# Kernel tuning notes

Measured on AMD Instinct MI355X. Metric: run time of the kernel, lower is better.

## Reference

```python
import jax, jax.numpy as jnp
import numpy as np

# --- dims (match init_kwargs) ---
H = 2048      # hidden_dim
NH = 16       # num_heads
QL = 1536     # q_latent_dim
KVL = 512     # kv_latent_dim
QR = 64       # q_rope_dim (== k_rope_dim)
QN = 128      # q_nope_dim
KR = 64       # k_rope_dim
KN = 128      # k_nope_dim
VD = 128      # v_dim
B, S = 1, 2048
BASE = 10000.0
EPS = 1e-6


def rms_norm(x, w, eps=EPS):
    xf = x.astype(jnp.float32)
    var = jnp.mean(xf * xf, axis=-1, keepdims=True)
    return w * (xf * jax.lax.rsqrt(var + eps)).astype(x.dtype)


def rope_cos_sin(seq_len, dim, base=BASE):
    inv_freq = 1.0 / (base ** (jnp.arange(0, dim, 2, dtype=jnp.float32) / dim))
    t = jnp.arange(seq_len, dtype=jnp.float32)
    freqs = jnp.outer(t, inv_freq)
    emb = jnp.concatenate([freqs, freqs], axis=-1)  # [S, dim]
    return jnp.cos(emb), jnp.sin(emb)


def rotate_half(x):
    d = x.shape[-1] // 2
    return jnp.concatenate([-x[..., d:], x[..., :d]], axis=-1)


def apply_rotary_pos_emb(q, k, cos, sin, position_ids):
    # cos/sin: [S, d]; position_ids: [B, S] -> [B, 1, S, d]
    cos = cos[position_ids][:, None]
    sin = sin[position_ids][:, None]

    def interleave(x):  # matches view(b,h,s,d//2,2).transpose(4,3).reshape
        b, h, s, d = x.shape
        return x.reshape(b, h, s, d // 2, 2).transpose(0, 1, 2, 4, 3).reshape(b, h, s, d)

    q = interleave(q)
    k = interleave(k)
    return q * cos + rotate_half(q) * sin, k * cos + rotate_half(k) * sin


def setup_inputs() -> dict:
    key = jax.random.key(0)
    ks = jax.random.split(key, 8)
    sc = 0.02
    hidden_states = jax.random.normal(ks[0], (B, S, H), dtype=jnp.float32)
    position_ids = jnp.broadcast_to(jnp.arange(S, dtype=jnp.int32), (B, S))
    attn_mask = jnp.tril(jnp.ones((S, S), dtype=jnp.int32))[None, None]  # causal, [1,1,S,S]
    return {
        "hidden_states": hidden_states,
        "position_ids": position_ids,
        "attn_mask": attn_mask,
        "q_down_w": jax.random.normal(ks[1], (QL, H), jnp.float32) * sc,
        "kv_down_w": jax.random.normal(ks[2], (KVL + KR, H), jnp.float32) * sc,
        "q_up_w": jax.random.normal(ks[3], (NH * (QN + QR), QL), jnp.float32) * sc,
        "k_up_w": jax.random.normal(ks[4], (NH * (KN + VD), KVL), jnp.float32) * sc,
        "o_w": jax.random.normal(ks[5], (H, NH * VD), jnp.float32) * sc,
        "q_norm_w": jnp.ones((QL,), jnp.float32),
        "kv_norm_w": jnp.ones((KVL + KR,), jnp.float32),
    }


def reference(hidden_states, position_ids, attn_mask, q_down_w, kv_down_w,
              q_up_w, k_up_w, o_w, q_norm_w, kv_norm_w):
    bsz, seq_len, _ = hidden_states.shape

    # --- query path: down-proj -> RMSNorm -> up-proj ---
    latent_cq = rms_norm(hidden_states @ q_down_w.T, q_norm_w)        # [B,S,QL]
    q = latent_cq @ q_up_w.T                                          # [B,S,NH*(QN+QR)]
    q = q.reshape(bsz, seq_len, NH, QN + QR).transpose(0, 2, 1, 3)    # [B,NH,S,QN+QR]
    q_nope, q_pe = q[..., :QN], q[..., QN:]

    # --- kv path: down-proj -> RMSNorm -> split latent / shared k_pe ---
    compressed_kv = rms_norm(hidden_states @ kv_down_w.T, kv_norm_w)  # [B,S,KVL+KR]
    latent_ckv, k_pe = compressed_kv[..., :KVL], compressed_kv[..., KVL:]
    kv = latent_ckv @ k_up_w.T                                        # [B,S,NH*(KN+VD)]
    kv = kv.reshape(bsz, seq_len, NH, KN + VD).transpose(0, 2, 1, 3)  # [B,NH,S,KN+VD]
    k_nope, value = kv[..., :KN], kv[..., KN:]

    # --- partial RoPE on rotary sub-dims ---
    cos, sin = rope_cos_sin(seq_len, QR)
    k_pe = k_pe[:, None]                                              # [B,1,S,KR] shared across heads
    q_rope, k_rope = apply_rotary_pos_emb(q_pe, k_pe, cos, sin, position_ids)
    k_rope = jnp.broadcast_to(k_rope, (bsz, NH, seq_len, KR))

    query = jnp.concatenate([q_rope, q_nope], axis=-1)                # [B,NH,S,QR+QN]
    key = jnp.concatenate([k_rope, k_nope], axis=-1)                  # [B,NH,S,KR+KN]

    # --- explicit attention (no 1/sqrt(d) scale, matching the source) ---
    attn_weights = jnp.einsum('bhqd,bhkd->bhqk', query, key)
    attn_weights = jnp.where(attn_mask == 0, -jnp.inf, attn_weights)
    attn_weights = jax.nn.softmax(attn_weights, axis=-1)
    attn_output = jnp.einsum('bhqk,bhkd->bhqd', attn_weights, value)
    attn_output = attn_output.transpose(0, 2, 1, 3).reshape(bsz, seq_len, NH * VD)
    attn_output = attn_output @ o_w.T                                 # [B,S,H]
    return attn_weights, attn_output
```

## Files before the change

### kernel.cpp

```cpp
#include <hip/hip_runtime.h>
#include <cstdint>
#include <cmath>

typedef _Float16 f16;
using f16x8 = __attribute__((ext_vector_type(8))) _Float16;
using f16x4 = __attribute__((ext_vector_type(4))) _Float16;
using f32x4 = __attribute__((ext_vector_type(4))) float;

#define NHEAD 16
#define SEQ   2048
#define KSS   4
#define NEG_INF -3.0e38f

static __device__ __forceinline__ f32x4 mfma16(f16x8 a, f16x8 b, f32x4 c) {
    return __builtin_amdgcn_mfma_f32_16x16x32_f16(a, b, c, 0, 0, 0);
}

static __device__ __forceinline__ void gload16(const void* gp, void* lp) {
    __builtin_amdgcn_global_load_lds(
        (const __attribute__((address_space(1))) unsigned int*)gp,
        (__attribute__((address_space(3))) unsigned int*)lp, 16, 0, 0);
}

__global__ __launch_bounds__(256) void k_cvt_all(
    const float* __restrict__ hsrc, const float* __restrict__ qdw, const float* __restrict__ kvdw,
    const float* __restrict__ quw, const float* __restrict__ kuw, const float* __restrict__ ow,
    f16* __restrict__ h16, f16* __restrict__ dw16, f16* __restrict__ quw16,
    f16* __restrict__ kuw16, f16* __restrict__ ow16, float* __restrict__ cs)
{
    constexpr int C1 = 1048576;
    constexpr int C2 = C1 + 786432;
    constexpr int C3 = C2 + 327680;
    constexpr int C4 = C3 + 1179648;
    constexpr int C5 = C4 + 524288;
    constexpr int C6 = C5 + 1048576;
    int chunk = blockIdx.x * 256 + threadIdx.x;
    if (chunk >= C6) {
        int idx = chunk - C6;
        if (idx < 65536) {
            int t = idx >> 5, j = idx & 31;
            float invf = (float)pow(10000.0, -(double)j / 32.0);
            float ang  = (float)t * invf;
            cs[t * 64 + j]      = (float)cos((double)ang);
            cs[t * 64 + 32 + j] = (float)sin((double)ang);
        }
        return;
    }
    const float* src; f16* dst; int off; int nvalid;
    if (chunk < C1)      { src = hsrc; dst = h16;  off = chunk;      nvalid = 4194304; }
    else if (chunk < C2) { src = qdw;  dst = dw16; off = chunk - C1; nvalid = 3145728; }
    else if (chunk < C3) { src = kvdw; dst = dw16 + 3145728; off = chunk - C2; nvalid = 1179648; }
    else if (chunk < C4) { src = quw;  dst = quw16; off = chunk - C3; nvalid = 4718592; }
    else if (chunk < C5) { src = kuw;  dst = kuw16; off = chunk - C4; nvalid = 2097152; }
    else                 { src = ow;   dst = ow16;  off = chunk - C5; nvalid = 4194304; }
    int i = off * 4;
    f16x4 o;
#pragma unroll
    for (int k = 0; k < 4; k++) {
        int idx = i + k;
        float v = (idx < nvalid) ? src[idx] : 0.f;
        o[k] = (f16)v;
    }
    *(f16x4*)&dst[i] = o;
}

template <typename OutT, bool NT>
static __device__ __forceinline__ void gemm_body(const f16* __restrict__ A, const f16* __restrict__ B,
                                                 OutT* __restrict__ C, int K, int ldc,
                                                 int m0, int n0, int k0, int k1,
                                                 f16* __restrict__ lds)
{
    const int tid  = threadIdx.x;
    const int lane = tid & 63;
    const int wv   = tid >> 6;
    const int l15  = lane & 15;
    const int lg   = lane >> 4;
    const int wm   = (wv >> 1) * 64;
    const int wn   = (wv & 1) * 64;

    f32x4 acc[4][4] = {};

    f16* As = lds;
    f16* Bs = lds + 8192;

    const int srow = tid >> 3;
    const int g    = (tid & 7) ^ (srow & 7);
    const f16* ap = &A[(size_t)(m0 + srow) * K + g * 8];
    const f16* bp = &B[(size_t)(n0 + srow) * K + g * 8];
    const int ldst = wv * 512;

    for (int kt = k0; kt < k1; kt += 64) {
        __syncthreads();
#pragma unroll
        for (int p = 0; p < 4; p++) {
            gload16(ap + (size_t)(p * 32) * K + kt, As + p * 2048 + ldst);
            gload16(bp + (size_t)(p * 32) * K + kt, Bs + p * 2048 + ldst);
        }
        __syncthreads();
#pragma unroll
        for (int ki = 0; ki < 2; ki++) {
            f16x8 af[4], bf[4];
#pragma unroll
            for (int i = 0; i < 4; i++) {
                const int ar = wm + i * 16 + l15;
                af[i] = *(const f16x8*)&As[ar * 64 + (((ki * 4 + lg) ^ (ar & 7)) << 3)];
            }
#pragma unroll
            for (int i = 0; i < 4; i++) {
                const int br = wn + i * 16 + l15;
                bf[i] = *(const f16x8*)&Bs[br * 64 + (((ki * 4 + lg) ^ (br & 7)) << 3)];
            }
#pragma unroll
            for (int i = 0; i < 4; i++)
#pragma unroll
                for (int j = 0; j < 4; j++)
                    acc[i][j] = mfma16(af[i], bf[j], acc[i][j]);
        }
    }
#pragma unroll
    for (int i = 0; i < 4; i++) {
#pragma unroll
        for (int j = 0; j < 4; j++) {
            const int row = m0 + wm + i * 16 + lg * 4;
            const int col = n0 + wn + j * 16 + l15;
#pragma unroll
            for (int r = 0; r < 4; r++) {
                if constexpr (NT)
                    __builtin_nontemporal_store((OutT)acc[i][j][r], &C[(size_t)(row + r) * ldc + col]);
                else
                    C[(size_t)(row + r) * ldc + col] = (OutT)acc[i][j][r];
            }
        }
    }
}

template <typename OutT, bool NT, int SPLITK>
__global__ __launch_bounds__(256) void k_gemm(const f16* __restrict__ A, const f16* __restrict__ B,
                                              OutT* __restrict__ C, int K, int ldc, size_t zstride)
{
    __shared__ __align__(16) f16 lds[16384];
    const int ks   = (SPLITK > 1) ? (int)blockIdx.z : 0;
    const int ksub = K / SPLITK;
    gemm_body<OutT, NT>(A, B, C + (size_t)ks * zstride, K, ldc,
                        blockIdx.y * 128, blockIdx.x * 128, ks * ksub, ks * ksub + ksub, lds);
}

__global__ __launch_bounds__(256) void k_up_fused(const f16* __restrict__ cq, const f16* __restrict__ quw,
                                                  f16* __restrict__ q_all,
                                                  const f16* __restrict__ lat, const f16* __restrict__ kuw,
                                                  f16* __restrict__ kv_all)
{
    __shared__ __align__(16) f16 lds[16384];
    if (blockIdx.x < 24)
        gemm_body<f16, false>(cq, quw, q_all, 1536, 3072,
                              blockIdx.y * 128, blockIdx.x * 128, 0, 1536, lds);
    else
        gemm_body<f16, false>(lat, kuw, kv_all, 512, 4096,
                              blockIdx.y * 128, (blockIdx.x - 24) * 128, 0, 512, lds);
}

__global__ __launch_bounds__(256) void k_add2f(const f16* __restrict__ p, float* __restrict__ out)
{
    size_t i = ((size_t)blockIdx.x * 256 + threadIdx.x) * 8;
    f16x8 a = *(const f16x8*)&p[i];
    f16x8 b = *(const f16x8*)&p[(size_t)2048 * 2048 + i];
    f32x4 o0, o1;
#pragma unroll
    for (int k = 0; k < 4; k++) {
        o0[k] = (float)a[k] + (float)b[k];
        o1[k] = (float)a[k + 4] + (float)b[k + 4];
    }
    __builtin_nontemporal_store(o0, (f32x4*)&out[i]);
    __builtin_nontemporal_store(o1, (f32x4*)&out[i + 4]);
}

__global__ __launch_bounds__(256) void k_rms_both(const f16* __restrict__ P0, const f16* __restrict__ P1,
                                                  const float* __restrict__ wq, const float* __restrict__ wkv,
                                                  f16* __restrict__ cq, f16* __restrict__ lat,
                                                  f16* __restrict__ kro, const float* __restrict__ cs)
{
    const int row = blockIdx.x, tid = threadIdx.x;
    const f16* a = &P0[(size_t)row * 2176];
    const f16* b = &P1[(size_t)row * 2176];

    float v0[8], v1[8];
    float ssq = 0.f, ssk = 0.f;
    {
        f16x8 a8 = *(const f16x8*)&a[tid * 8];
        f16x8 b8 = *(const f16x8*)&b[tid * 8];
#pragma unroll
        for (int e = 0; e < 8; e++) {
            float v = (float)a8[e] + (float)b8[e];
            v0[e] = v;
            if (tid < 192) ssq += v * v; else ssk += v * v;
        }
    }
    if (tid < 8) {
        const int cc = 256 + tid;
        f16x8 a8 = *(const f16x8*)&a[cc * 8];
        f16x8 b8 = *(const f16x8*)&b[cc * 8];
#pragma unroll
        for (int e = 0; e < 8; e++) {
            float v = (float)a8[e] + (float)b8[e];
            v1[e] = v;
            ssk += v * v;
        }
    }
#pragma unroll
    for (int off = 32; off > 0; off >>= 1) {
        ssq += __shfl_xor(ssq, off);
        ssk += __shfl_xor(ssk, off);
    }
    __shared__ float part[4][2];
    if ((tid & 63) == 0) { part[tid >> 6][0] = ssq; part[tid >> 6][1] = ssk; }
    __syncthreads();
    float totq = part[0][0] + part[1][0] + part[2][0] + part[3][0];
    float totk = part[0][1] + part[1][1] + part[2][1] + part[3][1];
    float scq = 1.f / sqrtf(totq / 1536.f + 1e-6f);
    float sck = 1.f / sqrtf(totk / 576.f + 1e-6f);

    if (tid < 192) {
        f16x8 o;
#pragma unroll
        for (int e = 0; e < 8; e++) o[e] = (f16)(wq[tid * 8 + e] * v0[e] * scq);
        *(f16x8*)&cq[(size_t)row * 1536 + tid * 8] = o;
    } else {
        const int lc = (tid - 192) * 8;
        f16x8 o;
#pragma unroll
        for (int e = 0; e < 8; e++) o[e] = (f16)(wkv[lc + e] * v0[e] * sck);
        *(f16x8*)&lat[(size_t)row * 512 + lc] = o;
    }
    if (tid < 8) {
        float t[8];
#pragma unroll
        for (int e = 0; e < 8; e++) t[e] = wkv[512 + tid * 8 + e] * v1[e] * sck;
        const int j0 = tid * 4;
        f16x4 oc, os;
#pragma unroll
        for (int e2 = 0; e2 < 4; e2++) {
            const int j = j0 + e2;
            float cv = cs[row * 64 + j], sv = cs[row * 64 + 32 + j];
            oc[e2] = (f16)(t[2 * e2] * cv - t[2 * e2 + 1] * sv);
            os[e2] = (f16)(t[2 * e2 + 1] * cv + t[2 * e2] * sv);
        }
        *(f16x4*)&kro[row * 64 + j0]      = oc;
        *(f16x4*)&kro[row * 64 + 32 + j0] = os;
    }
}

__global__ __launch_bounds__(256) void k_asm_all(const f16* __restrict__ q_all, const float* __restrict__ cs,
                                                 f16* __restrict__ Qf,
                                                 const f16* __restrict__ kv_all,
                                                 f16* __restrict__ Knope,
                                                 f16* __restrict__ Vt)
{
    __shared__ __align__(16) f16 Vs[128][136];
    const int tid = threadIdx.x;

    if (blockIdx.x < 3072) {
        const int gid = blockIdx.x * 256 + tid;
        const int p   = gid % 24;
        const int rowi = gid / 24;
        const int h = rowi >> 11, s = rowi & 2047;
        const f16* qrow = &q_all[(size_t)s * 3072 + h * 192];
        f16x8 o;
        if (p < 8) {
            const int pp = (p < 4) ? p : (p - 4);
            f16x8 la = *(const f16x8*)&qrow[128 + 16 * pp];
            f16x8 lb = *(const f16x8*)&qrow[136 + 16 * pp];
            const float* cb = &cs[s * 64 + 8 * pp];
#pragma unroll
            for (int e = 0; e < 8; e++) {
                float av = (float)((e < 4) ? la[2 * e] : lb[2 * e - 8]);
                float bv = (float)((e < 4) ? la[2 * e + 1] : lb[2 * e - 7]);
                float cv = cb[e], sv = cb[32 + e];
                o[e] = (f16)((p < 4) ? (av * cv - bv * sv) : (bv * cv + av * sv));
            }
        } else {
            o = *(const f16x8*)&qrow[8 * p - 64];
        }
        *(f16x8*)&Qf[((size_t)h * SEQ + s) * 192 + 8 * p] = o;
        return;
    }

    const int b  = blockIdx.x - 3072;
    const int s0 = (b & 15) * 128;
    const int h  = b >> 4;
#pragma unroll
    for (int i = 0; i < 16; i++) {
        const int c = tid + 256 * i;
        const int s_loc = c >> 5;
        const int g = c & 31;
        f16x8 v = *(const f16x8*)&kv_all[(size_t)(s0 + s_loc) * 4096 + h * 256 + g * 8];
        if (g < 16) {
            *(f16x8*)&Knope[((size_t)h * 2048 + s0 + s_loc) * 128 + g * 8] = v;
        } else {
            const int d0 = (g - 16) * 8;
#pragma unroll
            for (int k = 0; k < 8; k++) Vs[d0 + k][s_loc] = v[k];
        }
    }
    __syncthreads();
#pragma unroll
    for (int i = 0; i < 8; i++) {
        const int c = tid + 256 * i;
        const int d = c >> 4;
        const int gs = c & 15;
        f16x8 v = *(const f16x8*)&Vs[d][gs * 8];
        *(f16x8*)&Vt[((size_t)h * 128 + d) * 2048 + s0 + gs * 8] = v;
    }
}

__global__ __launch_bounds__(256) void k_stats(
    const f16* __restrict__ Qf, const f16* __restrict__ Krope, const f16* __restrict__ Knope,
    float* __restrict__ lpart)
{
    const int h  = blockIdx.z;
    const int ks = blockIdx.y;
    const int qt = blockIdx.x;
    const int q0 = qt * 64;
    const int tid = threadIdx.x;
    const int lane = tid & 63;
    const int wv = tid >> 6;
    const int l15 = lane & 15;
    const int lg  = lane >> 4;
    const int rowb = q0 + wv * 16;

    __shared__ __align__(16) f16 Ks_[64][200];

    float l[4] = {0.f, 0.f, 0.f, 0.f};

    if (ks <= qt) {
        f16x8 qf[6];
        {
            const f16* qbase = &Qf[((size_t)h * SEQ + rowb + l15) * 192];
#pragma unroll
            for (int kf = 0; kf < 6; kf++)
                qf[kf] = *(const f16x8*)&qbase[kf * 32 + lg * 8];
        }
        const int srow = tid >> 2;
        const int sp4  = tid & 3;
        const f32x4 vzero = {0.f, 0.f, 0.f, 0.f};

        for (int t = ks; t <= qt; t += KSS) {
            const int c0 = t * 64;
            __syncthreads();
#pragma unroll
            for (int i = 0; i < 6; i++) {
                const int p = sp4 + 4 * i;
                f16x8 v;
                if (p < 8) v = *(const f16x8*)&Krope[(size_t)(c0 + srow) * 64 + p * 8];
                else       v = *(const f16x8*)&Knope[((size_t)h * SEQ + c0 + srow) * 128 + (p - 8) * 8];
                *(f16x8*)&Ks_[srow][p * 8] = v;
            }
            __syncthreads();

            f32x4 s[4];
#pragma unroll
            for (int ni = 0; ni < 4; ni++) {
                s[ni] = vzero;
                const f16* kp = &Ks_[ni * 16 + l15][0];
#pragma unroll
                for (int kf = 0; kf < 6; kf++)
                    s[ni] = mfma16(qf[kf], *(const f16x8*)&kp[kf * 32 + lg * 8], s[ni]);
            }

#pragma unroll
            for (int ni = 0; ni < 4; ni++) {
                const int col = c0 + ni * 16 + l15;
#pragma unroll
                for (int r = 0; r < 4; r++) {
                    const int row = rowb + lg * 4 + r;
                    l[r] += (col <= row) ? __expf(s[ni][r]) : 0.f;
                }
            }
        }
#pragma unroll
        for (int off = 1; off < 16; off <<= 1)
#pragma unroll
            for (int r = 0; r < 4; r++)
                l[r] += __shfl_xor(l[r], off);
    }

    if (l15 == 0) {
#pragma unroll
        for (int r = 0; r < 4; r++) {
            const int rin = wv * 16 + lg * 4 + r;
            lpart[(((size_t)h * 32 + qt) * KSS + ks) * 64 + rin] = l[r];
        }
    }
}

__global__ __launch_bounds__(256) void k_pv(
    const f16* __restrict__ Qf, const f16* __restrict__ Krope, const f16* __restrict__ Knope,
    const f16* __restrict__ Vt, const float* __restrict__ lpart,
    float* __restrict__ attnw,
    f16* __restrict__ Ohead)
{
    const int h  = blockIdx.y;
    const int qt = (h >= 8) ? (31 - (int)blockIdx.x) : (int)blockIdx.x;
    const int q0 = qt * 64;
    const int tid = threadIdx.x;
    const int lane = tid & 63;
    const int wv = tid >> 6;
    const int l15 = lane & 15;
    const int lg  = lane >> 4;
    const int rowb = q0 + wv * 16;

    __shared__ __align__(16) f16 Ks_[64][200];
    __shared__ __align__(16) f16 Vs[128][72];
    __shared__ __align__(16) f16 Plds[4][16][72];

    f16x8 qf[6];
    {
        const f16* qbase = &Qf[((size_t)h * SEQ + rowb + l15) * 192];
#pragma unroll
        for (int kf = 0; kf < 6; kf++)
            qf[kf] = *(const f16x8*)&qbase[kf * 32 + lg * 8];
    }

    float rlr[4];
    {
        const float* base = &lpart[(((size_t)h * 32 + qt) * KSS) * 64];
#pragma unroll
        for (int r = 0; r < 4; r++) {
            const int rin = wv * 16 + lg * 4 + r;
            float ll = 0.f;
#pragma unroll
            for (int k2 = 0; k2 < KSS; k2++) ll += base[k2 * 64 + rin];
            rlr[r] = 1.f / ll;
        }
    }

    f32x4 o[8] = {};
    const f32x4 vzero = {0.f, 0.f, 0.f, 0.f};
    const int srow = tid >> 2;
    const int sp4  = tid & 3;

    for (int t = 0; t <= qt; t++) {
        const int c0 = t * 64;
        __syncthreads();
#pragma unroll
        for (int i = 0; i < 6; i++) {
            const int p = sp4 + 4 * i;
            f16x8 v;
            if (p < 8) v = *(const f16x8*)&Krope[(size_t)(c0 + srow) * 64 + p * 8];
            else       v = *(const f16x8*)&Knope[((size_t)h * SEQ + c0 + srow) * 128 + (p - 8) * 8];
            *(f16x8*)&Ks_[srow][p * 8] = v;
        }
#pragma unroll
        for (int i = 0; i < 4; i++) {
            const int c = tid + 256 * i;
            const int d = c >> 3, x = c & 7;
            *(f16x8*)&Vs[d][x * 8] = *(const f16x8*)&Vt[((size_t)h * 128 + d) * SEQ + c0 + x * 8];
        }
        __syncthreads();

        f32x4 s[4];
#pragma unroll
        for (int ni = 0; ni < 4; ni++) {
            s[ni] = vzero;
            const f16* kp = &Ks_[ni * 16 + l15][0];
#pragma unroll
            for (int kf = 0; kf < 6; kf++)
                s[ni] = mfma16(qf[kf], *(const f16x8*)&kp[kf * 32 + lg * 8], s[ni]);
        }

#pragma unroll
        for (int ni = 0; ni < 4; ni++) {
            const int col = c0 + ni * 16 + l15;
#pragma unroll
            for (int r = 0; r < 4; r++) {
                const int row = rowb + lg * 4 + r;
                float p = (col <= row) ? __expf(s[ni][r]) * rlr[r] : 0.f;
                __builtin_nontemporal_store(p, &attnw[((size_t)h * SEQ + row) * SEQ + col]);
                Plds[wv][lg * 4 + r][ni * 16 + l15] = (f16)p;
            }
        }
        asm volatile("" ::: "memory");

        f16x8 pa0 = *(const f16x8*)&Plds[wv][l15][lg * 8];
        f16x8 pa1 = *(const f16x8*)&Plds[wv][l15][32 + lg * 8];
#pragma unroll
        for (int nd = 0; nd < 8; nd++) {
            const f16* vp = &Vs[nd * 16 + l15][lg * 8];
            o[nd] = mfma16(pa0, *(const f16x8*)&vp[0],  o[nd]);
            o[nd] = mfma16(pa1, *(const f16x8*)&vp[32], o[nd]);
        }
    }

#pragma unroll
    for (int nd = 0; nd < 8; nd++)
#pragma unroll
        for (int r = 0; r < 4; r++) {
            const int row = rowb + lg * 4 + r;
            Ohead[(size_t)row * 2048 + h * 128 + nd * 16 + l15] = (f16)o[nd][r];
        }

    {
        const int cstart = q0 + 64;
        const int zc = SEQ - cstart;
        if (zc > 0) {
            const int nchunk = zc >> 2;
            for (int i = tid; i < 64 * nchunk; i += 256) {
                const int r  = i / nchunk;
                const int cc = (i - r * nchunk) << 2;
                __builtin_nontemporal_store(vzero,
                    (f32x4*)&attnw[((size_t)h * SEQ + q0 + r) * SEQ + cstart + cc]);
            }
        }
    }
}

extern "C" void kernel_launch(void* const* d_in, const int* in_sizes, int n_in,
                              void* d_out, int out_size, void* d_ws, size_t ws_size,
                              hipStream_t stream)
{
    (void)in_sizes; (void)n_in; (void)out_size; (void)ws_size;
    const float* hidden    = (const float*)d_in[0];
    const float* q_down_w  = (const float*)d_in[3];
    const float* kv_down_w = (const float*)d_in[4];
    const float* q_up_w    = (const float*)d_in[5];
    const float* k_up_w    = (const float*)d_in[6];
    const float* o_w       = (const float*)d_in[7];
    const float* q_norm_w  = (const float*)d_in[8];
    const float* kv_norm_w = (const float*)d_in[9];

    float* attnw = (float*)d_out;
    float* outp  = attnw + (size_t)NHEAD * SEQ * SEQ;

    char* wp = (char*)d_ws;
    auto aws = [&](size_t bytes) { void* p = (void*)wp; wp += (bytes + 255) & ~(size_t)255; return p; };
    f16*  ow16  = (f16*)aws((size_t)2048 * 2048 * 2);
    f16*  Ohead = (f16*)aws((size_t)2048 * 2048 * 2);
    f16*  Qf    = (f16*)aws((size_t)16 * 2048 * 192 * 2);
    f16*  Knope = (f16*)aws((size_t)16 * 2048 * 128 * 2);
    f16*  Vt    = (f16*)aws((size_t)16 * 128 * 2048 * 2);
    f16*  Krope = (f16*)aws((size_t)2048 * 64 * 2);
    float* cs   = (float*)aws((size_t)2048 * 64 * 4);
    float* lpart  = (float*)aws((size_t)16 * 32 * KSS * 64 * 4);
    f16*  opp    = (f16*)Qf;

    char* sp = (char*)d_out;
    auto aso = [&](size_t bytes) { void* p = (void*)sp; sp += (bytes + 255) & ~(size_t)255; return p; };
    f16*  h16      = (f16*)aso((size_t)2048 * 2048 * 2);
    f16*  dw16     = (f16*)aso((size_t)2176 * 2048 * 2);
    f16*  quw16    = (f16*)aso((size_t)3072 * 1536 * 2);
    f16*  kuw16    = (f16*)aso((size_t)4096 * 512 * 2);
    f16*  down_part = (f16*)aso((size_t)2 * 2048 * 2176 * 2);
    f16*  cq16     = (f16*)aso((size_t)2048 * 1536 * 2);
    f16*  latent16 = (f16*)aso((size_t)2048 * 512 * 2);
    f16*  q_all    = (f16*)aso((size_t)2048 * 3072 * 2);
    f16*  kv_all   = (f16*)aso((size_t)2048 * 4096 * 2);

    k_cvt_all<<<dim3(19456), dim3(256), 0, stream>>>(
        hidden, q_down_w, kv_down_w, q_up_w, k_up_w, o_w,
        h16, dw16, quw16, kuw16, ow16, cs);

    k_gemm<f16, false, 2><<<dim3(17, 16, 2), dim3(256), 0, stream>>>(
        h16, dw16, down_part, 2048, 2176, (size_t)2048 * 2176);

    k_rms_both<<<dim3(2048), dim3(256), 0, stream>>>(
        down_part, down_part + (size_t)2048 * 2176, q_norm_w, kv_norm_w,
        cq16, latent16, Krope, cs);

    k_up_fused<<<dim3(56, 16), dim3(256), 0, stream>>>(cq16, quw16, q_all, latent16, kuw16, kv_all);

    k_asm_all<<<dim3(3072 + 256), dim3(256), 0, stream>>>(q_all, cs, Qf, kv_all, Knope, Vt);

    k_stats<<<dim3(32, KSS, 16), dim3(256), 0, stream>>>(Qf, Krope, Knope, lpart);
    k_pv<<<dim3(32, 16), dim3(256), 0, stream>>>(Qf, Krope, Knope, Vt, lpart, attnw, Ohead);

    k_gemm<f16, false, 2><<<dim3(16, 16, 2), dim3(256), 0, stream>>>(
        Ohead, ow16, opp, 2048, 2048, (size_t)2048 * 2048);
    k_add2f<<<dim3(2048), dim3(256), 0, stream>>>(opp, outp);
}
```

Measured before the change: 323.5 us.

## Double-buffer GEMM LDS tiles and simplify causal zero-fill indexing

The shared GEMM body now uses two LDS buffers, issuing the global-to-LDS loads for the next K tile while MFMAs run on the current one. This halves the barriers per K step and hides load latency, at the cost of doubling LDS per block (64 KB), which may lower occupancy. The zero-fill of the masked upper triangle of the attention weights now assigns each thread a fixed row with strided columns, replacing the per-element divide. The unrolled pair loop assumes K per split is a multiple of 128.

```diff
diff --git a/kernel.cpp b/kernel.cpp
--- a/kernel.cpp
+++ b/kernel.cpp
@@ -80,8 +80,10 @@
 
     f32x4 acc[4][4] = {};
 
-    f16* As = lds;
-    f16* Bs = lds + 8192;
+    f16* As0 = lds;
+    f16* Bs0 = lds + 8192;
+    f16* As1 = lds + 16384;
+    f16* Bs1 = lds + 24576;
 
     const int srow = tid >> 3;
     const int g    = (tid & 7) ^ (srow & 7);
@@ -89,26 +91,26 @@
     const f16* bp = &B[(size_t)(n0 + srow) * K + g * 8];
     const int ldst = wv * 512;
 
-    for (int kt = k0; kt < k1; kt += 64) {
-        __syncthreads();
+    auto stage = [&](int kt, f16* Asb, f16* Bsb) {
 #pragma unroll
         for (int p = 0; p < 4; p++) {
-            gload16(ap + (size_t)(p * 32) * K + kt, As + p * 2048 + ldst);
-            gload16(bp + (size_t)(p * 32) * K + kt, Bs + p * 2048 + ldst);
-        }
-        __syncthreads();
+            gload16(ap + (size_t)(p * 32) * K + kt, Asb + p * 2048 + ldst);
+            gload16(bp + (size_t)(p * 32) * K + kt, Bsb + p * 2048 + ldst);
+        }
+    };
+    auto compute = [&](const f16* Asb, const f16* Bsb) {
 #pragma unroll
         for (int ki = 0; ki < 2; ki++) {
             f16x8 af[4], bf[4];
 #pragma unroll
             for (int i = 0; i < 4; i++) {
                 const int ar = wm + i * 16 + l15;
-                af[i] = *(const f16x8*)&As[ar * 64 + (((ki * 4 + lg) ^ (ar & 7)) << 3)];
+                af[i] = *(const f16x8*)&Asb[ar * 64 + (((ki * 4 + lg) ^ (ar & 7)) << 3)];
             }
 #pragma unroll
             for (int i = 0; i < 4; i++) {
                 const int br = wn + i * 16 + l15;
-                bf[i] = *(const f16x8*)&Bs[br * 64 + (((ki * 4 + lg) ^ (br & 7)) << 3)];
+                bf[i] = *(const f16x8*)&Bsb[br * 64 + (((ki * 4 + lg) ^ (br & 7)) << 3)];
             }
 #pragma unroll
             for (int i = 0; i < 4; i++)
@@ -116,6 +118,17 @@
                 for (int j = 0; j < 4; j++)
                     acc[i][j] = mfma16(af[i], bf[j], acc[i][j]);
         }
+    };
+
+    stage(k0, As0, Bs0);
+    __syncthreads();
+    for (int kt = k0; kt < k1; kt += 128) {
+        stage(kt + 64, As1, Bs1);
+        compute(As0, Bs0);
+        __syncthreads();
+        if (kt + 128 < k1) stage(kt + 128, As0, Bs0);
+        compute(As1, Bs1);
+        __syncthreads();
     }
 #pragma unroll
     for (int i = 0; i < 4; i++) {
@@ -138,7 +151,7 @@
 __global__ __launch_bounds__(256) void k_gemm(const f16* __restrict__ A, const f16* __restrict__ B,
                                               OutT* __restrict__ C, int K, int ldc, size_t zstride)
 {
-    __shared__ __align__(16) f16 lds[16384];
+    __shared__ __align__(16) f16 lds[32768];
     const int ks   = (SPLITK > 1) ? (int)blockIdx.z : 0;
     const int ksub = K / SPLITK;
     gemm_body<OutT, NT>(A, B, C + (size_t)ks * zstride, K, ldc,
@@ -150,7 +163,7 @@
                                                   const f16* __restrict__ lat, const f16* __restrict__ kuw,
                                                   f16* __restrict__ kv_all)
 {
-    __shared__ __align__(16) f16 lds[16384];
+    __shared__ __align__(16) f16 lds[32768];
     if (blockIdx.x < 24)
         gemm_body<f16, false>(cq, quw, q_all, 1536, 3072,
                               blockIdx.y * 128, blockIdx.x * 128, 0, 1536, lds);
@@ -500,15 +513,13 @@
 
     {
         const int cstart = q0 + 64;
-        const int zc = SEQ - cstart;
-        if (zc > 0) {
-            const int nchunk = zc >> 2;
-            for (int i = tid; i < 64 * nchunk; i += 256) {
-                const int r  = i / nchunk;
-                const int cc = (i - r * nchunk) << 2;
-                __builtin_nontemporal_store(vzero,
-                    (f32x4*)&attnw[((size_t)h * SEQ + q0 + r) * SEQ + cstart + cc]);
-            }
+        const int nchunk = (SEQ - cstart) >> 2;
+        if (nchunk > 0) {
+            const int zr = tid >> 2;
+            const int zc0 = tid & 3;
+            float* rowp = &attnw[((size_t)h * SEQ + q0 + zr) * SEQ + cstart];
+            for (int cc = zc0; cc < nchunk; cc += 4)
+                __builtin_nontemporal_store(vzero, (f32x4*)&rowp[cc * 4]);
         }
     }
 }
```

New measurement: 343.7 us. +6.2%, slower.
